# Optimization experiments

Hardware: AMD Instinct MI355X
Metric: run time of the kernel (lower is better)

The kernel has to match this reference:

```python
import jax, jax.numpy as jnp
import numpy as np

M, N_ATOMS, N_BONDS, MAX_NB = 96, 96, 96, 3
HB = 158        # bond hidden size; linear is 2*HB -> HB
F_ATOM = 133    # unused by forward, present in signature


def _glorot(key, shape):
    fan_in = shape[1]
    return (jax.random.normal(key, shape, jnp.float32) / np.float32(np.sqrt(fan_in)))


def setup_inputs() -> dict:
    key = jax.random.key(0)
    ks = jax.random.split(key, 12)
    return {
        "a2b_": jax.random.randint(ks[0], (M, N_ATOMS, MAX_NB), 1, N_BONDS + 1, dtype=jnp.int32),
        "b2a_": jax.random.randint(ks[1], (M, N_BONDS), 0, N_ATOMS, dtype=jnp.int32),
        "b2revb_": jax.random.randint(ks[2], (M, N_BONDS), 0, N_BONDS, dtype=jnp.int32),
        "f_bonds_": jax.random.normal(ks[3], (M, N_BONDS, HB), jnp.float32),
        "f_atoms_": jax.random.normal(ks[4], (M, N_ATOMS, F_ATOM), jnp.float32),
        "bond_sum_": jnp.zeros((M, HB), jnp.float32),
        "W0": _glorot(ks[5], (HB, 2 * HB)), "b0": jnp.zeros((HB,), jnp.float32),
        "W1": _glorot(ks[6], (110, HB)),    "b1": jnp.zeros((110,), jnp.float32),
        "W2": _glorot(ks[7], (70, 110)),    "b2": jnp.zeros((70,), jnp.float32),
        "W3": _glorot(ks[8], (35, 70)),     "b3": jnp.zeros((35,), jnp.float32),
        "W4": _glorot(ks[9], (1, 35)),      "b4": jnp.zeros((1,), jnp.float32),
    }


def _message_pass(f_bonds, bond_sum, a2b, b2a, b2revb, W0, b0):
    # Faithful sequential replay of the nested python loops for one molecule.
    # f_bonds[c] is overwritten inside the inner loop (torch row view aliases),
    # and bond_sum carries across both loops -> single scan over (c, j) pairs.
    cs = jnp.repeat(jnp.arange(N_BONDS), MAX_NB)
    js = jnp.tile(jnp.arange(MAX_NB), N_BONDS)

    def step(carry, cj):
        fb, bs = carry
        c, j = cj
        d = a2b[b2a[c], j]                      # neighbor bond index (>=1 by construction)
        bs = fb[d - 1] + bs
        bs = bs - fb[b2revb[c]]
        nf = jnp.concatenate([fb[c], bs]) @ W0.T + b0   # 316 -> 158
        fb = fb.at[c].set(nf)
        return (fb, bs), None

    (fb, _), _ = jax.lax.scan(step, (f_bonds, bond_sum), (cs, js))
    return fb.sum(axis=0)                       # [HB]


def reference(a2b_, b2a_, b2revb_, f_bonds_, f_atoms_, bond_sum_,
              W0, b0, W1, b1, W2, b2, W3, b3, W4, b4):
    # f_atoms_ is accepted but never used, exactly as in the source module.
    mp = jax.vmap(_message_pass, in_axes=(0, 0, 0, 0, 0, None, None))(
        f_bonds_, bond_sum_, a2b_, b2a_, b2revb_, W0, b0)   # [M, HB]
    # Dropout layers are identity in eval mode. No activation after layer1 (per source).
    h = mp @ W1.T + b1
    h = jax.nn.relu(h @ W2.T + b2)
    h = jax.nn.relu(h @ W3.T + b3)
    out = h @ W4.T + b4                                    # [M, 1]
    return out.reshape(-1)                                 # cat of [1]-tensors -> [M]
```

## Files before the change

### kernel.cpp

```cpp
#include <hip/hip_runtime.h>

#define NBOND 96
#define HBS 158
#define NSTEP 288

__global__ __launch_bounds__(320, 2)
void gcn_mp_kernel(const int* __restrict__ a2b,
                   const int* __restrict__ b2a,
                   const int* __restrict__ b2revb,
                   const float* __restrict__ f_bonds,
                   const float* __restrict__ bond_sum,
                   const float* __restrict__ W0,
                   const float* __restrict__ b0,
                   const float* __restrict__ W1, const float* __restrict__ b1,
                   const float* __restrict__ W2, const float* __restrict__ b2v,
                   const float* __restrict__ W3, const float* __restrict__ b3,
                   const float* __restrict__ W4, const float* __restrict__ b4,
                   float* __restrict__ out)
{
  const int m = blockIdx.x;
  const int t = threadIdx.x;

  __shared__ __align__(16) float fb[NBOND * 160];
  __shared__ __align__(16) float xv[320];
  __shared__ float bss[160];
  __shared__ float part[8 * 161];
  __shared__ float hbuf[128];
  __shared__ int sD[NSTEP];
  __shared__ int sR[NSTEP];

  for (int idx = t; idx < NBOND * 160; idx += 320) {
    int r = idx / 160, o = idx - r * 160;
    fb[idx] = (o < HBS) ? f_bonds[(m * NBOND + r) * HBS + o] : 0.f;
  }
  if (t < 160) bss[t] = (t < HBS) ? bond_sum[m * HBS + t] : 0.f;

  for (int i = t; i < NSTEP; i += 320) {
    int c = i / 3, j = i - c * 3;
    int a = b2a[m * NBOND + c];
    sD[i] = a2b[(m * NBOND + a) * 3 + j] - 1;
    sR[i] = b2revb[m * NBOND + c];
  }

  const int og = t >> 3;
  const int s  = t & 7;
  float w[4][40];
#pragma unroll
  for (int r = 0; r < 4; ++r) {
    const int o = og * 4 + r;
#pragma unroll
    for (int kk = 0; kk < 40; ++kk) {
      const int k = s * 40 + kk;
      const int col = (k < 160) ? k : (k - 2);
      const bool valid = (o < HBS) && ((k < 160) ? (k < HBS) : (k < 160 + HBS));
      w[r][kk] = valid ? W0[o * (2 * HBS) + col] : 0.f;
    }
  }

  __syncthreads();

#pragma unroll 1
  for (int i = 0; i < NSTEP; ++i) {
    const int c = i / 3;
    const int dm1 = sD[i];
    const int rv  = sR[i];

    if (t < 160) {
      float b = bss[t] + fb[dm1 * 160 + t] - fb[rv * 160 + t];
      bss[t] = b;
      xv[160 + t] = b;
    } else {
      const int tt = t - 160;
      xv[tt] = fb[c * 160 + tt];
    }
    __syncthreads();

    float a0 = 0.f, a1 = 0.f, a2 = 0.f, a3 = 0.f;
    const float4* xq = (const float4*)(xv + s * 40);
#pragma unroll
    for (int q = 0; q < 10; ++q) {
      const float4 xx = xq[q];
      a0 = fmaf(w[0][4*q+0], xx.x, a0);
      a1 = fmaf(w[1][4*q+0], xx.x, a1);
      a2 = fmaf(w[2][4*q+0], xx.x, a2);
      a3 = fmaf(w[3][4*q+0], xx.x, a3);
      a0 = fmaf(w[0][4*q+1], xx.y, a0);
      a1 = fmaf(w[1][4*q+1], xx.y, a1);
      a2 = fmaf(w[2][4*q+1], xx.y, a2);
      a3 = fmaf(w[3][4*q+1], xx.y, a3);
      a0 = fmaf(w[0][4*q+2], xx.z, a0);
      a1 = fmaf(w[1][4*q+2], xx.z, a1);
      a2 = fmaf(w[2][4*q+2], xx.z, a2);
      a3 = fmaf(w[3][4*q+2], xx.z, a3);
      a0 = fmaf(w[0][4*q+3], xx.w, a0);
      a1 = fmaf(w[1][4*q+3], xx.w, a1);
      a2 = fmaf(w[2][4*q+3], xx.w, a2);
      a3 = fmaf(w[3][4*q+3], xx.w, a3);
    }
    const int pb = s * 161 + og * 4;
    part[pb + 0] = a0; part[pb + 1] = a1; part[pb + 2] = a2; part[pb + 3] = a3;
    __syncthreads();

    if (t < HBS) {
      float sum = b0[t];
#pragma unroll
      for (int ss = 0; ss < 8; ++ss) sum += part[ss * 161 + t];
      fb[c * 160 + t] = sum;
    }
    __syncthreads();
  }

  if (t < 160) {
    float acc = 0.f;
#pragma unroll 1
    for (int r = 0; r < NBOND; ++r) acc += fb[r * 160 + t];
    xv[t] = acc;
  }
  __syncthreads();

  if (t < 110) {
    float acc = b1[t];
    for (int o = 0; o < HBS; ++o) acc = fmaf(xv[o], W1[t * HBS + o], acc);
    hbuf[t] = acc;
  }
  __syncthreads();
  if (t < 70) {
    float acc = b2v[t];
    for (int k = 0; k < 110; ++k) acc = fmaf(hbuf[k], W2[t * 110 + k], acc);
    part[t] = fmaxf(acc, 0.f);
  }
  __syncthreads();
  if (t < 35) {
    float acc = b3[t];
    for (int k = 0; k < 70; ++k) acc = fmaf(part[k], W3[t * 70 + k], acc);
    xv[200 + t] = fmaxf(acc, 0.f);
  }
  __syncthreads();
  if (t == 0) {
    float acc = b4[0];
    for (int k = 0; k < 35; ++k) acc = fmaf(xv[200 + k], W4[k], acc);
    out[m] = acc;
  }
}

extern "C" void kernel_launch(void* const* d_in, const int* in_sizes, int n_in,
                              void* d_out, int out_size, void* d_ws, size_t ws_size,
                              hipStream_t stream)
{
  const int*   a2b      = (const int*)d_in[0];
  const int*   b2a      = (const int*)d_in[1];
  const int*   b2revb   = (const int*)d_in[2];
  const float* f_bonds  = (const float*)d_in[3];
  const float* bond_sum = (const float*)d_in[5];
  const float* W0 = (const float*)d_in[6];
  const float* b0 = (const float*)d_in[7];
  const float* W1 = (const float*)d_in[8];
  const float* b1 = (const float*)d_in[9];
  const float* W2 = (const float*)d_in[10];
  const float* b2 = (const float*)d_in[11];
  const float* W3 = (const float*)d_in[12];
  const float* b3 = (const float*)d_in[13];
  const float* W4 = (const float*)d_in[14];
  const float* b4 = (const float*)d_in[15];

  gcn_mp_kernel<<<dim3(96), dim3(320), 0, stream>>>(
      a2b, b2a, b2revb, f_bonds, bond_sum,
      W0, b0, W1, b1, W2, b2, W3, b3, W4, b4,
      (float*)d_out);
}
```

Baseline: 259.5 us.

## Split W0 matvec over 640 threads and reduce partials with wave shuffles

Doubles the block to 640 threads so each thread holds one output row's quarter of W0 (80 weights). Partial dot products are combined with two xor-shuffles inside a wave instead of going through shared memory. This removes one __syncthreads and the shared-memory reduction pass from each of the 288 sequential steps. In exchange it uses more threads per block, may raise register pressure, and lengthens each thread's FMA chain.

Result: slower. 267.5 us (+3.1%).

```diff
diff --git a/kernel.cpp b/kernel.cpp
--- a/kernel.cpp
+++ b/kernel.cpp
@@ -3,8 +3,9 @@
 #define NBOND 96
 #define HBS 158
 #define NSTEP 288
+#define NT 640
 
-__global__ __launch_bounds__(320, 2)
+__global__ __launch_bounds__(NT, 1)
 void gcn_mp_kernel(const int* __restrict__ a2b,
                    const int* __restrict__ b2a,
                    const int* __restrict__ b2revb,
@@ -24,121 +25,122 @@
   __shared__ __align__(16) float fb[NBOND * 160];
   __shared__ __align__(16) float xv[320];
   __shared__ float bss[160];
-  __shared__ float part[8 * 161];
-  __shared__ float hbuf[128];
+  __shared__ float hb1[112];
+  __shared__ float hb2[72];
+  __shared__ float hb3[40];
   __shared__ int sD[NSTEP];
   __shared__ int sR[NSTEP];
+  __shared__ int sC[NSTEP];
 
-  for (int idx = t; idx < NBOND * 160; idx += 320) {
+  for (int idx = t; idx < NBOND * 160; idx += NT) {
     int r = idx / 160, o = idx - r * 160;
     fb[idx] = (o < HBS) ? f_bonds[(m * NBOND + r) * HBS + o] : 0.f;
   }
   if (t < 160) bss[t] = (t < HBS) ? bond_sum[m * HBS + t] : 0.f;
 
-  for (int i = t; i < NSTEP; i += 320) {
+  if (t < NSTEP) {
+    int i = t;
     int c = i / 3, j = i - c * 3;
     int a = b2a[m * NBOND + c];
     sD[i] = a2b[(m * NBOND + a) * 3 + j] - 1;
     sR[i] = b2revb[m * NBOND + c];
+    sC[i] = c;
   }
 
-  const int og = t >> 3;
-  const int s  = t & 7;
-  float w[4][40];
+  const int o  = t >> 2;
+  const int kq = t & 3;
+  float w[80];
 #pragma unroll
-  for (int r = 0; r < 4; ++r) {
-    const int o = og * 4 + r;
-#pragma unroll
-    for (int kk = 0; kk < 40; ++kk) {
-      const int k = s * 40 + kk;
-      const int col = (k < 160) ? k : (k - 2);
-      const bool valid = (o < HBS) && ((k < 160) ? (k < HBS) : (k < 160 + HBS));
-      w[r][kk] = valid ? W0[o * (2 * HBS) + col] : 0.f;
-    }
+  for (int kk = 0; kk < 80; ++kk) {
+    const int k = kq * 80 + kk;
+    const int col = (k < 160) ? k : (k - 2);
+    const bool valid = (o < HBS) && ((k < 160) ? (k < HBS) : (k < 160 + HBS));
+    w[kk] = valid ? W0[o * (2 * HBS) + col] : 0.f;
   }
+  const float b0r = (kq == 0 && o < HBS) ? b0[o] : 0.f;
 
   __syncthreads();
 
 #pragma unroll 1
   for (int i = 0; i < NSTEP; ++i) {
-    const int c = i / 3;
-    const int dm1 = sD[i];
-    const int rv  = sR[i];
+    const int c = sC[i];
 
     if (t < 160) {
-      float b = bss[t] + fb[dm1 * 160 + t] - fb[rv * 160 + t];
+      float b = bss[t] + fb[sD[i] * 160 + t] - fb[sR[i] * 160 + t];
       bss[t] = b;
       xv[160 + t] = b;
-    } else {
+    } else if (t < 320) {
       const int tt = t - 160;
       xv[tt] = fb[c * 160 + tt];
     }
     __syncthreads();
 
-    float a0 = 0.f, a1 = 0.f, a2 = 0.f, a3 = 0.f;
-    const float4* xq = (const float4*)(xv + s * 40);
+    float acc0 = 0.f, acc1 = 0.f, acc2 = 0.f, acc3 = 0.f;
+    const float4* xq = (const float4*)(xv + kq * 80);
 #pragma unroll
-    for (int q = 0; q < 10; ++q) {
-      const float4 xx = xq[q];
-      a0 = fmaf(w[0][4*q+0], xx.x, a0);
-      a1 = fmaf(w[1][4*q+0], xx.x, a1);
-      a2 = fmaf(w[2][4*q+0], xx.x, a2);
-      a3 = fmaf(w[3][4*q+0], xx.x, a3);
-      a0 = fmaf(w[0][4*q+1], xx.y, a0);
-      a1 = fmaf(w[1][4*q+1], xx.y, a1);
-      a2 = fmaf(w[2][4*q+1], xx.y, a2);
-      a3 = fmaf(w[3][4*q+1], xx.y, a3);
-      a0 = fmaf(w[0][4*q+2], xx.z, a0);
-      a1 = fmaf(w[1][4*q+2], xx.z, a1);
-      a2 = fmaf(w[2][4*q+2], xx.z, a2);
-      a3 = fmaf(w[3][4*q+2], xx.z, a3);
-      a0 = fmaf(w[0][4*q+3], xx.w, a0);
-      a1 = fmaf(w[1][4*q+3], xx.w, a1);
-      a2 = fmaf(w[2][4*q+3], xx.w, a2);
-      a3 = fmaf(w[3][4*q+3], xx.w, a3);
+    for (int q = 0; q < 20; q += 4) {
+      const float4 x0 = xq[q + 0];
+      const float4 x1 = xq[q + 1];
+      const float4 x2 = xq[q + 2];
+      const float4 x3 = xq[q + 3];
+      acc0 = fmaf(w[4*q + 0],  x0.x, acc0);
+      acc0 = fmaf(w[4*q + 1],  x0.y, acc0);
+      acc0 = fmaf(w[4*q + 2],  x0.z, acc0);
+      acc0 = fmaf(w[4*q + 3],  x0.w, acc0);
+      acc1 = fmaf(w[4*q + 4],  x1.x, acc1);
+      acc1 = fmaf(w[4*q + 5],  x1.y, acc1);
+      acc1 = fmaf(w[4*q + 6],  x1.z, acc1);
+      acc1 = fmaf(w[4*q + 7],  x1.w, acc1);
+      acc2 = fmaf(w[4*q + 8],  x2.x, acc2);
+      acc2 = fmaf(w[4*q + 9],  x2.y, acc2);
+      acc2 = fmaf(w[4*q + 10], x2.z, acc2);
+      acc2 = fmaf(w[4*q + 11], x2.w, acc2);
+      acc3 = fmaf(w[4*q + 12], x3.x, acc3);
+      acc3 = fmaf(w[4*q + 13], x3.y, acc3);
+      acc3 = fmaf(w[4*q + 14], x3.z, acc3);
+      acc3 = fmaf(w[4*q + 15], x3.w, acc3);
     }
-    const int pb = s * 161 + og * 4;
-    part[pb + 0] = a0; part[pb + 1] = a1; part[pb + 2] = a2; part[pb + 3] = a3;
-    __syncthreads();
-
-    if (t < HBS) {
-      float sum = b0[t];
-#pragma unroll
-      for (int ss = 0; ss < 8; ++ss) sum += part[ss * 161 + t];
-      fb[c * 160 + t] = sum;
-    }
+    float acc = (acc0 + acc1) + (acc2 + acc3);
+    acc += __shfl_xor(acc, 1, 64);
+    acc += __shfl_xor(acc, 2, 64);
+    if (kq == 0) fb[c * 160 + o] = acc + b0r;
     __syncthreads();
   }
 
   if (t < 160) {
-    float acc = 0.f;
-#pragma unroll 1
-    for (int r = 0; r < NBOND; ++r) acc += fb[r * 160 + t];
-    xv[t] = acc;
+    float s0 = 0.f, s1 = 0.f, s2 = 0.f, s3 = 0.f;
+#pragma unroll
+    for (int r = 0; r < NBOND; r += 4) {
+      s0 += fb[(r + 0) * 160 + t];
+      s1 += fb[(r + 1) * 160 + t];
+      s2 += fb[(r + 2) * 160 + t];
+      s3 += fb[(r + 3) * 160 + t];
+    }
+    xv[t] = (s0 + s1) + (s2 + s3);
   }
   __syncthreads();
 
   if (t < 110) {
     float acc = b1[t];
-    for (int o = 0; o < HBS; ++o) acc = fmaf(xv[o], W1[t * HBS + o], acc);
-    hbuf[t] = acc;
+    for (int k = 0; k < HBS; ++k) acc = fmaf(xv[k], W1[t * HBS + k], acc);
+    hb1[t] = acc;
   }
   __syncthreads();
   if (t < 70) {
     float acc = b2v[t];
-    for (int k = 0; k < 110; ++k) acc = fmaf(hbuf[k], W2[t * 110 + k], acc);
-    part[t] = fmaxf(acc, 0.f);
+    for (int k = 0; k < 110; ++k) acc = fmaf(hb1[k], W2[t * 110 + k], acc);
+    hb2[t] = fmaxf(acc, 0.f);
   }
   __syncthreads();
   if (t < 35) {
     float acc = b3[t];
-    for (int k = 0; k < 70; ++k) acc = fmaf(part[k], W3[t * 70 + k], acc);
-    xv[200 + t] = fmaxf(acc, 0.f);
+    for (int k = 0; k < 70; ++k) acc = fmaf(hb2[k], W3[t * 70 + k], acc);
+    hb3[t] = fmaxf(acc, 0.f);
   }
   __syncthreads();
   if (t == 0) {
     float acc = b4[0];
-    for (int k = 0; k < 35; ++k) acc = fmaf(xv[200 + k], W4[k], acc);
+    for (int k = 0; k < 35; ++k) acc = fmaf(hb3[k], W4[k], acc);
     out[m] = acc;
   }
 }
@@ -163,7 +165,7 @@
   const float* W4 = (const float*)d_in[14];
   const float* b4 = (const float*)d_in[15];
 
-  gcn_mp_kernel<<<dim3(96), dim3(320), 0, stream>>>(
+  gcn_mp_kernel<<<dim3(96), dim3(NT), 0, stream>>>(
       a2b, b2a, b2revb, f_bonds, bond_sum,
       W0, b0, W1, b1, W2, b2, W3, b3, W4, b4,
       (float*)d_out);
```

## Cut per-step barriers with shuffle reduction and double-buffered next-step input prep

Applied to the files above, without the earlier changes.

Replaces the shared-memory partial-sum reduction with an in-wave xor-shuffle reduction across the 8 k-slices, so the reduced outputs stay in registers. Within the same step, a few lanes build the next step's input vector and running bond_sum in a double-buffered xv. Aliasing between the row just written and the next step's neighbor or reverse indices is handled with flag bits precomputed into the index tables. This leaves one barrier per sequential step instead of three, and the final row sum is accumulated in registers on each row's last update. The cost is more intricate lane-role logic and launch bounds relaxed to one block per CU.

Measured after the change: 302.5 us. 1.17x slower.

```diff
diff --git a/kernel.cpp b/kernel.cpp
--- a/kernel.cpp
+++ b/kernel.cpp
@@ -3,8 +3,9 @@
 #define NBOND 96
 #define HBS 158
 #define NSTEP 288
-
-__global__ __launch_bounds__(320, 2)
+#define NT 320
+
+__global__ __launch_bounds__(NT, 1)
 void gcn_mp_kernel(const int* __restrict__ a2b,
                    const int* __restrict__ b2a,
                    const int* __restrict__ b2revb,
@@ -18,36 +19,38 @@
                    const float* __restrict__ W4, const float* __restrict__ b4,
                    float* __restrict__ out)
 {
-  const int m = blockIdx.x;
-  const int t = threadIdx.x;
+  const int m  = blockIdx.x;
+  const int t  = threadIdx.x;
+  const int og = t >> 3;
+  const int s  = t & 7;
 
   __shared__ __align__(16) float fb[NBOND * 160];
-  __shared__ __align__(16) float xv[320];
-  __shared__ float bss[160];
-  __shared__ float part[8 * 161];
-  __shared__ float hbuf[128];
-  __shared__ int sD[NSTEP];
-  __shared__ int sR[NSTEP];
-
-  for (int idx = t; idx < NBOND * 160; idx += 320) {
+  __shared__ __align__(16) float xv[2][320];
+  __shared__ int sDp[NSTEP];
+  __shared__ int sRp[NSTEP];
+  __shared__ __align__(16) float mpb[160];
+  __shared__ float hb1[112], hb2[72], hb3[40];
+
+  for (int idx = t; idx < NBOND * 160; idx += NT) {
     int r = idx / 160, o = idx - r * 160;
     fb[idx] = (o < HBS) ? f_bonds[(m * NBOND + r) * HBS + o] : 0.f;
   }
-  if (t < 160) bss[t] = (t < HBS) ? bond_sum[m * HBS + t] : 0.f;
-
-  for (int i = t; i < NSTEP; i += 320) {
-    int c = i / 3, j = i - c * 3;
-    int a = b2a[m * NBOND + c];
-    sD[i] = a2b[(m * NBOND + a) * 3 + j] - 1;
-    sR[i] = b2revb[m * NBOND + c];
-  }
-
-  const int og = t >> 3;
-  const int s  = t & 7;
+  if (t < NSTEP) {
+    int i = t, c = i / 3, j = i - 3 * c;
+    int a  = b2a[m * NBOND + c];
+    int d  = a2b[(m * NBOND + a) * 3 + j] - 1;
+    int rv = b2revb[m * NBOND + c];
+    int cp = (i == 0) ? -1 : (i - 1) / 3;
+    sDp[i] = d  | ((d  == cp) ? 0x10000 : 0);
+    sRp[i] = rv | ((rv == cp) ? 0x10000 : 0);
+  }
+
   float w[4][40];
+  float b0r[4];
 #pragma unroll
   for (int r = 0; r < 4; ++r) {
     const int o = og * 4 + r;
+    b0r[r] = (o < HBS) ? b0[o] : 0.f;
 #pragma unroll
     for (int kk = 0; kk < 40; ++kk) {
       const int k = s * 40 + kk;
@@ -56,89 +59,122 @@
       w[r][kk] = valid ? W0[o * (2 * HBS) + col] : 0.f;
     }
   }
-
-  __syncthreads();
+  __syncthreads();
+
+  if (t < 160) {
+    int d0 = sDp[0] & 0xFFFF, r0 = sRp[0] & 0xFFFF;
+    xv[0][t] = fb[t];
+    float bsv = ((t < HBS) ? bond_sum[m * HBS + t] : 0.f)
+              + fb[d0 * 160 + t] - fb[r0 * 160 + t];
+    xv[0][160 + t] = bsv;
+  }
+  __syncthreads();
+
+  float cs0 = 0.f, cs1 = 0.f, cs2 = 0.f, cs3 = 0.f;
+  int p = 0;
 
 #pragma unroll 1
   for (int i = 0; i < NSTEP; ++i) {
-    const int c = i / 3;
-    const int dm1 = sD[i];
-    const int rv  = sR[i];
-
-    if (t < 160) {
-      float b = bss[t] + fb[dm1 * 160 + t] - fb[rv * 160 + t];
-      bss[t] = b;
-      xv[160 + t] = b;
-    } else {
-      const int tt = t - 160;
-      xv[tt] = fb[c * 160 + tt];
-    }
+    const int c  = i / 3;
+    const int j  = i - 3 * c;
+    const int i1 = i + 1;
+    const int c1 = i1 / 3;
+    const int j1 = i1 - 3 * c1;
+    const bool hn = (i1 < NSTEP);
+
+    const float4* xp = (const float4*)(&xv[p][s * 40]);
+    float4 x0 = xp[0], x1 = xp[1], x2 = xp[2], x3 = xp[3], x4 = xp[4];
+    float4 x5 = xp[5], x6 = xp[6], x7 = xp[7], x8 = xp[8], x9 = xp[9];
+
+    float4 nxr = make_float4(0.f, 0.f, 0.f, 0.f);
+    float2 dd = make_float2(0.f, 0.f), rr = make_float2(0.f, 0.f), bo = make_float2(0.f, 0.f);
+    int aD = 0, aR = 0, e0 = 0;
+    if (hn) {
+      if (s == 1 && j1 == 0) {
+        nxr = *(const float4*)(&fb[c1 * 160 + og * 4]);
+      }
+      if (s >= 2 && s <= 3) {
+        const int pd = sDp[i1], pr = sRp[i1];
+        const int d  = pd & 0xFFFF;  aD = pd >> 16;
+        const int rv = pr & 0xFFFF;  aR = pr >> 16;
+        e0 = og * 4 + (s - 2) * 2;
+        dd = *(const float2*)(&fb[d  * 160 + e0]);
+        rr = *(const float2*)(&fb[rv * 160 + e0]);
+        bo = *(const float2*)(&xv[p][160 + e0]);
+      }
+    }
+
+    float a0 = 0.f, a1 = 0.f, a2 = 0.f, a3 = 0.f;
+#define QSTEP(qq, xx) \
+    a0 = fmaf(w[0][4*qq+0], xx.x, a0); a1 = fmaf(w[1][4*qq+0], xx.x, a1); \
+    a2 = fmaf(w[2][4*qq+0], xx.x, a2); a3 = fmaf(w[3][4*qq+0], xx.x, a3); \
+    a0 = fmaf(w[0][4*qq+1], xx.y, a0); a1 = fmaf(w[1][4*qq+1], xx.y, a1); \
+    a2 = fmaf(w[2][4*qq+1], xx.y, a2); a3 = fmaf(w[3][4*qq+1], xx.y, a3); \
+    a0 = fmaf(w[0][4*qq+2], xx.z, a0); a1 = fmaf(w[1][4*qq+2], xx.z, a1); \
+    a2 = fmaf(w[2][4*qq+2], xx.z, a2); a3 = fmaf(w[3][4*qq+2], xx.z, a3); \
+    a0 = fmaf(w[0][4*qq+3], xx.w, a0); a1 = fmaf(w[1][4*qq+3], xx.w, a1); \
+    a2 = fmaf(w[2][4*qq+3], xx.w, a2); a3 = fmaf(w[3][4*qq+3], xx.w, a3);
+    QSTEP(0, x0) QSTEP(1, x1) QSTEP(2, x2) QSTEP(3, x3) QSTEP(4, x4)
+    QSTEP(5, x5) QSTEP(6, x6) QSTEP(7, x7) QSTEP(8, x8) QSTEP(9, x9)
+#undef QSTEP
+
+    a0 += __shfl_xor(a0, 1); a0 += __shfl_xor(a0, 2); a0 += __shfl_xor(a0, 4);
+    a1 += __shfl_xor(a1, 1); a1 += __shfl_xor(a1, 2); a1 += __shfl_xor(a1, 4);
+    a2 += __shfl_xor(a2, 1); a2 += __shfl_xor(a2, 2); a2 += __shfl_xor(a2, 4);
+    a3 += __shfl_xor(a3, 1); a3 += __shfl_xor(a3, 2); a3 += __shfl_xor(a3, 4);
+    a0 += b0r[0]; a1 += b0r[1]; a2 += b0r[2]; a3 += b0r[3];
+
+    if (s == 0) {
+      *(float4*)(&fb[c * 160 + og * 4]) = make_float4(a0, a1, a2, a3);
+    }
+    if (hn) {
+      if (s == 1) {
+        float4 wv = (j1 == 0) ? nxr : make_float4(a0, a1, a2, a3);
+        *(float4*)(&xv[p ^ 1][og * 4]) = wv;
+      }
+      if (s >= 2 && s <= 3) {
+        float sA = (s == 2) ? a0 : a2;
+        float sB = (s == 2) ? a1 : a3;
+        float vd0 = aD ? sA : dd.x;
+        float vd1 = aD ? sB : dd.y;
+        float vr0 = aR ? sA : rr.x;
+        float vr1 = aR ? sB : rr.y;
+        *(float2*)(&xv[p ^ 1][160 + e0]) =
+            make_float2(bo.x + vd0 - vr0, bo.y + vd1 - vr1);
+      }
+    }
+    if (j == 2) { cs0 += a0; cs1 += a1; cs2 += a2; cs3 += a3; }
+
+    p ^= 1;
     __syncthreads();
-
-    float a0 = 0.f, a1 = 0.f, a2 = 0.f, a3 = 0.f;
-    const float4* xq = (const float4*)(xv + s * 40);
-#pragma unroll
-    for (int q = 0; q < 10; ++q) {
-      const float4 xx = xq[q];
-      a0 = fmaf(w[0][4*q+0], xx.x, a0);
-      a1 = fmaf(w[1][4*q+0], xx.x, a1);
-      a2 = fmaf(w[2][4*q+0], xx.x, a2);
-      a3 = fmaf(w[3][4*q+0], xx.x, a3);
-      a0 = fmaf(w[0][4*q+1], xx.y, a0);
-      a1 = fmaf(w[1][4*q+1], xx.y, a1);
-      a2 = fmaf(w[2][4*q+1], xx.y, a2);
-      a3 = fmaf(w[3][4*q+1], xx.y, a3);
-      a0 = fmaf(w[0][4*q+2], xx.z, a0);
-      a1 = fmaf(w[1][4*q+2], xx.z, a1);
-      a2 = fmaf(w[2][4*q+2], xx.z, a2);
-      a3 = fmaf(w[3][4*q+2], xx.z, a3);
-      a0 = fmaf(w[0][4*q+3], xx.w, a0);
-      a1 = fmaf(w[1][4*q+3], xx.w, a1);
-      a2 = fmaf(w[2][4*q+3], xx.w, a2);
-      a3 = fmaf(w[3][4*q+3], xx.w, a3);
-    }
-    const int pb = s * 161 + og * 4;
-    part[pb + 0] = a0; part[pb + 1] = a1; part[pb + 2] = a2; part[pb + 3] = a3;
-    __syncthreads();
-
-    if (t < HBS) {
-      float sum = b0[t];
-#pragma unroll
-      for (int ss = 0; ss < 8; ++ss) sum += part[ss * 161 + t];
-      fb[c * 160 + t] = sum;
-    }
-    __syncthreads();
-  }
-
-  if (t < 160) {
-    float acc = 0.f;
-#pragma unroll 1
-    for (int r = 0; r < NBOND; ++r) acc += fb[r * 160 + t];
-    xv[t] = acc;
+  }
+
+  if (s == 0) {
+    *(float4*)(&mpb[og * 4]) = make_float4(cs0, cs1, cs2, cs3);
   }
   __syncthreads();
 
   if (t < 110) {
     float acc = b1[t];
-    for (int o = 0; o < HBS; ++o) acc = fmaf(xv[o], W1[t * HBS + o], acc);
-    hbuf[t] = acc;
+    for (int k = 0; k < HBS; ++k) acc = fmaf(mpb[k], W1[t * HBS + k], acc);
+    hb1[t] = acc;
   }
   __syncthreads();
   if (t < 70) {
     float acc = b2v[t];
-    for (int k = 0; k < 110; ++k) acc = fmaf(hbuf[k], W2[t * 110 + k], acc);
-    part[t] = fmaxf(acc, 0.f);
+    for (int k = 0; k < 110; ++k) acc = fmaf(hb1[k], W2[t * 110 + k], acc);
+    hb2[t] = fmaxf(acc, 0.f);
   }
   __syncthreads();
   if (t < 35) {
     float acc = b3[t];
-    for (int k = 0; k < 70; ++k) acc = fmaf(part[k], W3[t * 70 + k], acc);
-    xv[200 + t] = fmaxf(acc, 0.f);
+    for (int k = 0; k < 70; ++k) acc = fmaf(hb2[k], W3[t * 70 + k], acc);
+    hb3[t] = fmaxf(acc, 0.f);
   }
   __syncthreads();
   if (t == 0) {
     float acc = b4[0];
-    for (int k = 0; k < 35; ++k) acc = fmaf(xv[200 + k], W4[k], acc);
+    for (int k = 0; k < 35; ++k) acc = fmaf(hb3[k], W4[k], acc);
     out[m] = acc;
   }
 }
@@ -163,7 +199,7 @@
   const float* W4 = (const float*)d_in[14];
   const float* b4 = (const float*)d_in[15];
 
-  gcn_mp_kernel<<<dim3(96), dim3(320), 0, stream>>>(
+  gcn_mp_kernel<<<dim3(96), dim3(NT), 0, stream>>>(
       a2b, b2a, b2revb, f_bonds, bond_sum,
       W0, b0, W1, b1, W2, b2, W3, b3, W4, b4,
       (float*)d_out);
```
